# Kernel tuning notes

Measured on AMD Instinct MI355X. Metric: run time of the kernel, lower is better.

Reference implementation:

```python
import jax, jax.numpy as jnp
import numpy as np


def monarch_linear(x, w1, w2, bias, out_features):
    """Monarch structured linear: permute + block-diag + permute + block-diag.
    x: (B, n_in); w1: (k, q, p); w2: (l, s, r) with k*q == l*r.
    """
    b, n = x.shape
    k, q, p = w1.shape
    l, s, r = w2.shape
    n_ext = k * p
    if n_ext > n:  # preprocess: zero-pad input to in_features_extended
        x = jnp.pad(x, ((0, 0), (0, n_ext - n)))
    # first block-diagonal matmul: (B,k,p) x (k,q,p) -> (B,k,q)
    out1 = jnp.einsum('bkp,kqp->bkq', x.reshape(b, k, p), w1)
    # permutation: view (B, k*q) as (B, r, l) then transpose -> (B, l, r)
    out1 = out1.reshape(b, r, l).transpose(0, 2, 1)
    # second block-diagonal matmul: (B,l,r) x (l,s,r) -> (B,l,s)
    out2 = jnp.einsum('blr,lsr->bls', out1, w2)
    # final permutation: (B,l,s) -> (B,s,l) -> (B, s*l), then slice to out_features
    out = out2.transpose(0, 2, 1).reshape(b, s * l)[:, :out_features]
    return out + bias


def setup_inputs() -> dict:
    key = jax.random.key(0)
    ks = jax.random.split(key, 14)
    B = 65536
    specs = {
        'x': (B, 1, 28, 28),
        'fc1_w1': (15, 27, 53), 'fc1_w2': (15, 27, 27), 'fc1_b': (392,),
        'fc2_w1': (15, 9, 27), 'fc2_w2': (15, 9, 9), 'fc2_b': (128,),
        'fc3_w1': (15, 5, 9), 'fc3_w2': (15, 5, 5), 'fc3_b': (64,),
        'fc4_w1': (15, 1, 5), 'fc4_w2': (15, 1, 1), 'fc4_b': (10,),
    }
    out = {}
    for i, (name, shape) in enumerate(specs.items()):
        v = jax.random.normal(ks[i], shape, dtype=jnp.float32)
        if name != 'x':
            v = v * 0.1  # keep activations in a sane range through 4 layers
        out[name] = v
    return out


def reference(x, fc1_w1, fc1_w2, fc1_b, fc2_w1, fc2_w2, fc2_b,
              fc3_w1, fc3_w2, fc3_b, fc4_w1, fc4_w2, fc4_b):
    gelu = lambda t: jax.nn.gelu(t, approximate=False)  # torch F.gelu default = exact erf
    h = x.reshape(x.shape[0], -1)  # flatten (B,1,28,28) -> (B,784)
    h = gelu(monarch_linear(h, fc1_w1, fc1_w2, fc1_b, 392))
    h = gelu(monarch_linear(h, fc2_w1, fc2_w2, fc2_b, 128))
    h = gelu(monarch_linear(h, fc3_w1, fc3_w2, fc3_b, 64))
    h = monarch_linear(h, fc4_w1, fc4_w2, fc4_b, 10)
    return jax.nn.log_softmax(h, axis=1)
```

## Files before the change

kernel.cpp:

```cpp
#include <hip/hip_runtime.h>
#include <hip/hip_bf16.h>

typedef unsigned short u16;
typedef unsigned int   u32;

__device__ __forceinline__ float b2f(u16 v){ return __uint_as_float(((u32)v) << 16); }
__device__ __forceinline__ u16   f2b(float f){
  u32 u = __float_as_uint(f);
  u += 0x7fffu + ((u >> 16) & 1u);
  return (u16)(u >> 16);
}
__device__ __forceinline__ float gelu_exact(float x){
  return 0.5f * x * (1.0f + erff(x * 0.70710678118654752440f));
}

#define WTG_OFF   0
#define W2G_OFF   22720
#define W12G_OFF  34112
#define PREP_F    37952

__global__ __launch_bounds__(256) void k_prep(
    const float* __restrict__ w1, const float* __restrict__ w2,
    const float* __restrict__ w1_2, float* __restrict__ ws)
{
  int tid = blockIdx.x*256 + threadIdx.x;
  for (int e = tid; e < 15*54*28; e += gridDim.x*256){
    int kk = e / 1512, rem = e - kk*1512;
    int p = rem / 28, j = rem - p*28;
    ws[WTG_OFF + e] = (p < 53 && j < 27) ? w1[(kk*27 + j)*53 + p] : 0.0f;
  }
  for (int e = tid; e < 15*27*28; e += gridDim.x*256){
    int l = e / 756, rem = e - l*756;
    int s = rem / 28, r = rem - s*28;
    ws[W2G_OFF + e] = (r < 27) ? w2[(l*27 + s)*27 + r] : 0.0f;
  }
  for (int e = tid; e < 15*9*28; e += gridDim.x*256){
    int kk = e / 252, rem = e - kk*252;
    int j = rem / 28, p = rem - j*28;
    ws[W12G_OFF + e] = (p < 27) ? w1_2[(kk*9 + j)*27 + p] : 0.0f;
  }
}

__global__ __launch_bounds__(256, 5) void k_fc1a(
    const float* __restrict__ x, const float* __restrict__ wtg,
    u16* __restrict__ act, int base, int Bc)
{
  __shared__ u32 xsu[256*27];
  const int tid = threadIdx.x;
  const int k   = blockIdx.y;
  const int rowloc = blockIdx.x * 256;

  #pragma unroll 4
  for (int i = 0; i < 27; ++i){
    int e = i*256 + tid;
    int r = e / 27, c2 = e - r*27;
    int col = k*53 + 2*c2;
    const size_t rowoff = (size_t)(base + rowloc + r)*784;
    float v0 = 0.f, v1 = 0.f;
    if (col < 784) v0 = x[rowoff + col];
    if (2*c2+1 < 53 && col+1 < 784) v1 = x[rowoff + col + 1];
    xsu[e] = (u32)f2b(v0) | ((u32)f2b(v1) << 16);
  }
  __syncthreads();

  float acc[28];
  #pragma unroll
  for (int j = 0; j < 28; ++j) acc[j] = 0.0f;

  const float* __restrict__ wk = wtg + (size_t)k*1512;
  const u32* xrow = &xsu[tid*27];
  #pragma unroll
  for (int pp = 0; pp < 27; ++pp){
    const u32 xv2 = xrow[pp];
    const float x0 = __uint_as_float(xv2 << 16);
    const float x1 = __uint_as_float(xv2 & 0xffff0000u);
    const float4* wa = (const float4*)(wk + 56*pp);
    const float4* wb = (const float4*)(wk + 56*pp + 28);
    #pragma unroll
    for (int i = 0; i < 7; ++i){
      const float4 a = wa[i];
      const float4 b = wb[i];
      acc[4*i+0] = fmaf(a.x, x0, fmaf(b.x, x1, acc[4*i+0]));
      acc[4*i+1] = fmaf(a.y, x0, fmaf(b.y, x1, acc[4*i+1]));
      acc[4*i+2] = fmaf(a.z, x0, fmaf(b.z, x1, acc[4*i+2]));
      acc[4*i+3] = fmaf(a.w, x0, fmaf(b.w, x1, acc[4*i+3]));
    }
  }
  const int r0 = rowloc + tid;
  #pragma unroll
  for (int j = 0; j < 27; ++j)
    act[(size_t)(k*27 + j)*Bc + r0] = f2b(acc[j]);
}

__global__ __launch_bounds__(256) void k_fc1b(
    const float* __restrict__ w2g, const float* __restrict__ b1,
    u16* act, int Bc)
{
  const int tid = threadIdx.x;
  const int l   = blockIdx.y;
  const int row = blockIdx.x*256 + tid;
  const float* __restrict__ wl = w2g + (size_t)l*756;

  float t[28];
  #pragma unroll
  for (int r = 0; r < 27; ++r) t[r] = b2f(act[(size_t)(r*15 + l)*Bc + row]);
  t[27] = 0.0f;
  #pragma unroll
  for (int s = 0; s < 27; ++s){
    const float4* wp = (const float4*)(wl + s*28);
    float va = 0.f, vb = 0.f;
    #pragma unroll
    for (int i = 0; i < 7; ++i){
      const float4 w = wp[i];
      va = fmaf(w.x, t[4*i+0], va); vb = fmaf(w.y, t[4*i+1], vb);
      va = fmaf(w.z, t[4*i+2], va); vb = fmaf(w.w, t[4*i+3], vb);
    }
    const int m = s*15 + l;
    const float bb = (m < 392) ? b1[m] : 0.0f;
    const float h = (m < 392) ? gelu_exact(va + vb + bb) : 0.0f;
    act[(size_t)m*Bc + row] = f2b(h);
  }
}

__global__ __launch_bounds__(256) void k_fc2a(
    const u16* __restrict__ h1t, const float* __restrict__ w12g,
    u16* __restrict__ o2t, int Bc)
{
  const int tid = threadIdx.x;
  const int k   = blockIdx.y;
  const int row = blockIdx.x*256 + tid;
  const float* __restrict__ wk = w12g + (size_t)k*252;

  float hb[28];
  #pragma unroll
  for (int p = 0; p < 27; ++p) hb[p] = b2f(h1t[(size_t)(k*27 + p)*Bc + row]);
  hb[27] = 0.0f;
  #pragma unroll
  for (int j = 0; j < 9; ++j){
    const float4* wp = (const float4*)(wk + j*28);
    float va = 0.f, vb = 0.f;
    #pragma unroll
    for (int i = 0; i < 7; ++i){
      const float4 w = wp[i];
      va = fmaf(w.x, hb[4*i+0], va); vb = fmaf(w.y, hb[4*i+1], vb);
      va = fmaf(w.z, hb[4*i+2], va); vb = fmaf(w.w, hb[4*i+3], vb);
    }
    o2t[(size_t)(k*9 + j)*Bc + row] = f2b(va + vb);
  }
}

__global__ __launch_bounds__(256) void k_fc2b(
    const u16* __restrict__ o2t, const float* __restrict__ w2_2,
    const float* __restrict__ b2, u16* __restrict__ h2t, int Bc)
{
  const int tid = threadIdx.x;
  const int l   = blockIdx.y;
  const float* __restrict__ wl = w2_2 + (size_t)l*81;

  const int row = blockIdx.x*256 + tid;
  float t[9];
  #pragma unroll
  for (int r = 0; r < 9; ++r) t[r] = b2f(o2t[(size_t)(r*15 + l)*Bc + row]);
  #pragma unroll
  for (int s = 0; s < 9; ++s){
    float v = 0.f;
    #pragma unroll
    for (int r = 0; r < 9; ++r) v = fmaf(wl[s*9 + r], t[r], v);
    const int m = s*15 + l;
    float h = (m < 128) ? gelu_exact(v + b2[m < 128 ? m : 0]) : 0.0f;
    h2t[(size_t)m*Bc + row] = f2b(h);
  }
}

__global__ __launch_bounds__(256) void k_fc3a(
    const u16* __restrict__ h2t, const float* __restrict__ w1_3,
    u16* __restrict__ o3t, int Bc)
{
  const int tid = threadIdx.x;
  const int k   = blockIdx.y;
  const float* __restrict__ wk = w1_3 + (size_t)k*45;

  const int row = blockIdx.x*256 + tid;
  float hb[9];
  #pragma unroll
  for (int p = 0; p < 9; ++p) hb[p] = b2f(h2t[(size_t)(k*9 + p)*Bc + row]);
  #pragma unroll
  for (int j = 0; j < 5; ++j){
    float v = 0.f;
    #pragma unroll
    for (int p = 0; p < 9; ++p) v = fmaf(wk[j*9 + p], hb[p], v);
    o3t[(size_t)(k*5 + j)*Bc + row] = f2b(v);
  }
}

__global__ __launch_bounds__(256) void k_fc3b4(
    const u16* __restrict__ o3t,
    const float* __restrict__ w2_3, const float* __restrict__ b3,
    const float* __restrict__ w1_4, const float* __restrict__ w2_4, const float* __restrict__ b4,
    float* __restrict__ out, int base, int Bc)
{
  __shared__ float outS[256*10];
  const int tid = threadIdx.x;
  const int rloc = blockIdx.x*256 + tid;

  float sacc[10];
  #pragma unroll
  for (int c = 0; c < 10; ++c) sacc[c] = 0.0f;

  #pragma unroll
  for (int l = 0; l < 15; ++l){
    float t[5];
    #pragma unroll
    for (int r = 0; r < 5; ++r) t[r] = b2f(o3t[(size_t)(r*15 + l)*Bc + rloc]);
    #pragma unroll
    for (int s = 0; s < 5; ++s){
      const int m = s*15 + l;
      if (m < 50){
        const float* wp = w2_3 + (l*5 + s)*5;
        float v = 0.f;
        v = fmaf(wp[0], t[0], v); v = fmaf(wp[1], t[1], v);
        v = fmaf(wp[2], t[2], v); v = fmaf(wp[3], t[3], v);
        v = fmaf(wp[4], t[4], v);
        const float h = gelu_exact(v + b3[m]);
        const int c = m / 5, p = m - (m/5)*5;
        sacc[c] = fmaf(h, w1_4[c*5 + p], sacc[c]);
      }
    }
  }
  float v[10];
  #pragma unroll
  for (int c = 0; c < 10; ++c) v[c] = fmaf(sacc[c], w2_4[c], b4[c]);

  float mx = v[0];
  #pragma unroll
  for (int c = 1; c < 10; ++c) mx = fmaxf(mx, v[c]);
  float sum = 0.f;
  #pragma unroll
  for (int c = 0; c < 10; ++c) sum += expf(v[c] - mx);
  const float lse = mx + logf(sum);
  #pragma unroll
  for (int c = 0; c < 10; ++c) outS[tid*10 + c] = v[c] - lse;
  __syncthreads();
  const size_t blockOut = (size_t)(base + blockIdx.x*256) * 10;
  #pragma unroll
  for (int i = 0; i < 10; ++i){
    int e = i*256 + tid;
    out[blockOut + e] = outS[e];
  }
}

extern "C" void kernel_launch(void* const* d_in, const int* in_sizes, int n_in,
                              void* d_out, int out_size, void* d_ws, size_t ws_size,
                              hipStream_t stream)
{
  const float* x     = (const float*)d_in[0];
  const float* f1w1  = (const float*)d_in[1];
  const float* f1w2  = (const float*)d_in[2];
  const float* f1b   = (const float*)d_in[3];
  const float* f2w1  = (const float*)d_in[4];
  const float* f2w2  = (const float*)d_in[5];
  const float* f2b   = (const float*)d_in[6];
  const float* f3w1  = (const float*)d_in[7];
  const float* f3w2  = (const float*)d_in[8];
  const float* f3b   = (const float*)d_in[9];
  const float* f4w1  = (const float*)d_in[10];
  const float* f4w2  = (const float*)d_in[11];
  const float* f4b   = (const float*)d_in[12];
  const int B = in_sizes[0] / 784;
  (void)n_in; (void)out_size;

  const size_t prepBytes = (size_t)PREP_F * sizeof(float);
  float* wsF  = (float*)d_ws;
  u16*  wsAct = (u16*)((char*)d_ws + prepBytes);

  k_prep<<<dim3(32), 256, 0, stream>>>(f1w1, f1w2, f2w1, wsF);

  const float* wtg  = wsF + WTG_OFF;
  const float* w2g  = wsF + W2G_OFF;
  const float* w12g = wsF + W12G_OFF;

  const size_t perRow = 750 * sizeof(u16);
  int Rc = B;
  if (ws_size - prepBytes < (size_t)B * perRow){
    size_t rows = (ws_size - prepBytes) / perRow;
    Rc = (int)(rows & ~(size_t)511);
    if (Rc < 512) Rc = 512;
  }
  for (int base = 0; base < B; base += Rc){
    const int Bc = (B - base < Rc) ? (B - base) : Rc;
    u16* act = wsAct;
    u16* o2t = act + (size_t)405 * Bc;
    u16* h2t = o2t + (size_t)135 * Bc;
    u16* o3t = h2t + (size_t)135 * Bc;
    k_fc1a<<<dim3(Bc/256, 15), 256, 0, stream>>>(x, wtg, act, base, Bc);
    k_fc1b<<<dim3(Bc/256, 15), 256, 0, stream>>>(w2g, f1b, act, Bc);
    k_fc2a<<<dim3(Bc/256, 15), 256, 0, stream>>>(act, w12g, o2t, Bc);
    k_fc2b<<<dim3(Bc/256, 15), 256, 0, stream>>>(o2t, f2w2, f2b, h2t, Bc);
    k_fc3a<<<dim3(Bc/256, 15), 256, 0, stream>>>(h2t, f3w1, o3t, Bc);
    k_fc3b4<<<dim3(Bc/256), 256, 0, stream>>>(o3t, f3w2, f3b,
                                              f4w1, f4w2, f4b, (float*)d_out, base, Bc);
  }
}
```

Measured before the change: 462.1 us.

## Fuse fc2b, fc3a and fc3b/fc4 tail into a single per-row kernel

Result: slower. 505.7 us (+9.4%).

```diff
diff --git a/kernel.cpp b/kernel.cpp
--- a/kernel.cpp
+++ b/kernel.cpp
@@ -10,6 +10,7 @@
   u += 0x7fffu + ((u >> 16) & 1u);
   return (u16)(u >> 16);
 }
+__device__ __forceinline__ float bfrt(float f){ return b2f(f2b(f)); }
 __device__ __forceinline__ float gelu_exact(float x){
   return 0.5f * x * (1.0f + erff(x * 0.70710678118654752440f));
 }
@@ -149,59 +150,46 @@
   }
 }
 
-__global__ __launch_bounds__(256) void k_fc2b(
-    const u16* __restrict__ o2t, const float* __restrict__ w2_2,
-    const float* __restrict__ b2, u16* __restrict__ h2t, int Bc)
-{
-  const int tid = threadIdx.x;
-  const int l   = blockIdx.y;
-  const float* __restrict__ wl = w2_2 + (size_t)l*81;
-
-  const int row = blockIdx.x*256 + tid;
-  float t[9];
-  #pragma unroll
-  for (int r = 0; r < 9; ++r) t[r] = b2f(o2t[(size_t)(r*15 + l)*Bc + row]);
-  #pragma unroll
-  for (int s = 0; s < 9; ++s){
-    float v = 0.f;
-    #pragma unroll
-    for (int r = 0; r < 9; ++r) v = fmaf(wl[s*9 + r], t[r], v);
-    const int m = s*15 + l;
-    float h = (m < 128) ? gelu_exact(v + b2[m < 128 ? m : 0]) : 0.0f;
-    h2t[(size_t)m*Bc + row] = f2b(h);
-  }
-}
-
-__global__ __launch_bounds__(256) void k_fc3a(
-    const u16* __restrict__ h2t, const float* __restrict__ w1_3,
-    u16* __restrict__ o3t, int Bc)
-{
-  const int tid = threadIdx.x;
-  const int k   = blockIdx.y;
-  const float* __restrict__ wk = w1_3 + (size_t)k*45;
-
-  const int row = blockIdx.x*256 + tid;
-  float hb[9];
-  #pragma unroll
-  for (int p = 0; p < 9; ++p) hb[p] = b2f(h2t[(size_t)(k*9 + p)*Bc + row]);
-  #pragma unroll
-  for (int j = 0; j < 5; ++j){
-    float v = 0.f;
-    #pragma unroll
-    for (int p = 0; p < 9; ++p) v = fmaf(wk[j*9 + p], hb[p], v);
-    o3t[(size_t)(k*5 + j)*Bc + row] = f2b(v);
-  }
-}
-
-__global__ __launch_bounds__(256) void k_fc3b4(
-    const u16* __restrict__ o3t,
+__global__ __launch_bounds__(256) void k_tail(
+    const u16* __restrict__ o2t,
+    const float* __restrict__ w2_2, const float* __restrict__ b2,
+    const float* __restrict__ w1_3,
     const float* __restrict__ w2_3, const float* __restrict__ b3,
     const float* __restrict__ w1_4, const float* __restrict__ w2_4, const float* __restrict__ b4,
     float* __restrict__ out, int base, int Bc)
 {
   __shared__ float outS[256*10];
   const int tid = threadIdx.x;
-  const int rloc = blockIdx.x*256 + tid;
+  const int row = blockIdx.x*256 + tid;
+
+  float h2[135];
+  #pragma unroll
+  for (int l = 0; l < 15; ++l){
+    float t[9];
+    #pragma unroll
+    for (int r = 0; r < 9; ++r) t[r] = b2f(o2t[(size_t)(r*15 + l)*Bc + row]);
+    #pragma unroll
+    for (int s = 0; s < 9; ++s){
+      const int m = s*15 + l;
+      float v = 0.f;
+      #pragma unroll
+      for (int r = 0; r < 9; ++r) v = fmaf(w2_2[l*81 + s*9 + r], t[r], v);
+      const float h = (m < 128) ? gelu_exact(v + b2[m < 128 ? m : 0]) : 0.0f;
+      h2[m] = bfrt(h);
+    }
+  }
+
+  float o3[75];
+  #pragma unroll
+  for (int k2 = 0; k2 < 15; ++k2){
+    #pragma unroll
+    for (int j = 0; j < 5; ++j){
+      float v = 0.f;
+      #pragma unroll
+      for (int p = 0; p < 9; ++p) v = fmaf(w1_3[k2*45 + j*9 + p], h2[k2*9 + p], v);
+      o3[k2*5 + j] = bfrt(v);
+    }
+  }
 
   float sacc[10];
   #pragma unroll
@@ -211,7 +199,7 @@
   for (int l = 0; l < 15; ++l){
     float t[5];
     #pragma unroll
-    for (int r = 0; r < 5; ++r) t[r] = b2f(o3t[(size_t)(r*15 + l)*Bc + rloc]);
+    for (int r = 0; r < 5; ++r) t[r] = o3[r*15 + l];
     #pragma unroll
     for (int s = 0; s < 5; ++s){
       const int m = s*15 + l;
@@ -279,7 +267,7 @@
   const float* w2g  = wsF + W2G_OFF;
   const float* w12g = wsF + W12G_OFF;
 
-  const size_t perRow = 750 * sizeof(u16);
+  const size_t perRow = 540 * sizeof(u16);
   int Rc = B;
   if (ws_size - prepBytes < (size_t)B * perRow){
     size_t rows = (ws_size - prepBytes) / perRow;
@@ -290,14 +278,11 @@
     const int Bc = (B - base < Rc) ? (B - base) : Rc;
     u16* act = wsAct;
     u16* o2t = act + (size_t)405 * Bc;
-    u16* h2t = o2t + (size_t)135 * Bc;
-    u16* o3t = h2t + (size_t)135 * Bc;
     k_fc1a<<<dim3(Bc/256, 15), 256, 0, stream>>>(x, wtg, act, base, Bc);
     k_fc1b<<<dim3(Bc/256, 15), 256, 0, stream>>>(w2g, f1b, act, Bc);
     k_fc2a<<<dim3(Bc/256, 15), 256, 0, stream>>>(act, w12g, o2t, Bc);
-    k_fc2b<<<dim3(Bc/256, 15), 256, 0, stream>>>(o2t, f2w2, f2b, h2t, Bc);
-    k_fc3a<<<dim3(Bc/256, 15), 256, 0, stream>>>(h2t, f3w1, o3t, Bc);
-    k_fc3b4<<<dim3(Bc/256), 256, 0, stream>>>(o3t, f3w2, f3b,
-                                              f4w1, f4w2, f4b, (float*)d_out, base, Bc);
-  }
-}
+    k_tail<<<dim3(Bc/256), 256, 0, stream>>>(o2t, f2w2, f2b, f3w1,
+                                             f3w2, f3b, f4w1, f4w2, f4b,
+                                             (float*)d_out, base, Bc);
+  }
+}
```

## Use bf16 MFMA with hi/lo weight split for fc1 first block-diagonal matmul

Applied to the files above, without the earlier changes.

Result: slower. 484.9 us (+4.9%).

```diff
diff --git a/kernel.cpp b/kernel.cpp
--- a/kernel.cpp
+++ b/kernel.cpp
@@ -3,6 +3,8 @@
 
 typedef unsigned short u16;
 typedef unsigned int   u32;
+typedef __attribute__((ext_vector_type(8))) short short8;
+typedef __attribute__((ext_vector_type(4))) float f32x4;
 
 __device__ __forceinline__ float b2f(u16 v){ return __uint_as_float(((u32)v) << 16); }
 __device__ __forceinline__ u16   f2b(float f){
@@ -14,82 +16,110 @@
   return 0.5f * x * (1.0f + erff(x * 0.70710678118654752440f));
 }
 
-#define WTG_OFF   0
-#define W2G_OFF   22720
-#define W12G_OFF  34112
-#define PREP_F    37952
+#define W2G_OFF   0
+#define W12G_OFF  11340
+#define PREP_F    15120
+#define WFRAG_U16 61440
+#define PREP_BYTES (PREP_F*4 + WFRAG_U16*2)
 
 __global__ __launch_bounds__(256) void k_prep(
     const float* __restrict__ w1, const float* __restrict__ w2,
-    const float* __restrict__ w1_2, float* __restrict__ ws)
+    const float* __restrict__ w1_2, float* __restrict__ wsF,
+    u16* __restrict__ wfrag)
 {
   int tid = blockIdx.x*256 + threadIdx.x;
-  for (int e = tid; e < 15*54*28; e += gridDim.x*256){
-    int kk = e / 1512, rem = e - kk*1512;
-    int p = rem / 28, j = rem - p*28;
-    ws[WTG_OFF + e] = (p < 53 && j < 27) ? w1[(kk*27 + j)*53 + p] : 0.0f;
-  }
   for (int e = tid; e < 15*27*28; e += gridDim.x*256){
     int l = e / 756, rem = e - l*756;
     int s = rem / 28, r = rem - s*28;
-    ws[W2G_OFF + e] = (r < 27) ? w2[(l*27 + s)*27 + r] : 0.0f;
+    wsF[W2G_OFF + e] = (r < 27) ? w2[(l*27 + s)*27 + r] : 0.0f;
   }
   for (int e = tid; e < 15*9*28; e += gridDim.x*256){
     int kk = e / 252, rem = e - kk*252;
     int j = rem / 28, p = rem - j*28;
-    ws[W12G_OFF + e] = (p < 27) ? w1_2[(kk*9 + j)*27 + p] : 0.0f;
-  }
-}
-
-__global__ __launch_bounds__(256, 5) void k_fc1a(
-    const float* __restrict__ x, const float* __restrict__ wtg,
+    wsF[W12G_OFF + e] = (p < 27) ? w1_2[(kk*9 + j)*27 + p] : 0.0f;
+  }
+  for (int e = tid; e < 30720; e += gridDim.x*256){
+    int k  = e / 2048, rem = e - k*2048;
+    int s  = rem / 1024; rem -= s*1024;
+    int ct = rem / 512;  int sl = rem - ct*512;
+    int lane = sl / 8, i = sl - lane*8;
+    int p = s*32 + (lane >> 4)*8 + i;
+    int j = ct*16 + (lane & 15);
+    float wv = (p < 53 && j < 27) ? w1[(k*27 + j)*53 + p] : 0.0f;
+    u16 hi = f2b(wv);
+    u16 lo = f2b(wv - b2f(hi));
+    int bidx = (k*2 + s)*2 + ct;
+    wfrag[bidx*1024 + sl]       = hi;
+    wfrag[bidx*1024 + 512 + sl] = lo;
+  }
+}
+
+__global__ __launch_bounds__(256, 4) void k_fc1a(
+    const float* __restrict__ x, const u16* __restrict__ wfrag,
     u16* __restrict__ act, int base, int Bc)
 {
-  __shared__ u32 xsu[256*27];
+  __shared__ __align__(16) u16 xs[256*72];
   const int tid = threadIdx.x;
   const int k   = blockIdx.y;
   const int rowloc = blockIdx.x * 256;
 
+  u32* xsu = (u32*)xs;
   #pragma unroll 4
-  for (int i = 0; i < 27; ++i){
+  for (int i = 0; i < 36; ++i){
     int e = i*256 + tid;
-    int r = e / 27, c2 = e - r*27;
+    int r = e / 36, c2 = e - r*36;
     int col = k*53 + 2*c2;
     const size_t rowoff = (size_t)(base + rowloc + r)*784;
     float v0 = 0.f, v1 = 0.f;
-    if (col < 784) v0 = x[rowoff + col];
+    if (2*c2   < 53 && col   < 784) v0 = x[rowoff + col];
     if (2*c2+1 < 53 && col+1 < 784) v1 = x[rowoff + col + 1];
     xsu[e] = (u32)f2b(v0) | ((u32)f2b(v1) << 16);
   }
   __syncthreads();
 
-  float acc[28];
-  #pragma unroll
-  for (int j = 0; j < 28; ++j) acc[j] = 0.0f;
-
-  const float* __restrict__ wk = wtg + (size_t)k*1512;
-  const u32* xrow = &xsu[tid*27];
-  #pragma unroll
-  for (int pp = 0; pp < 27; ++pp){
-    const u32 xv2 = xrow[pp];
-    const float x0 = __uint_as_float(xv2 << 16);
-    const float x1 = __uint_as_float(xv2 & 0xffff0000u);
-    const float4* wa = (const float4*)(wk + 56*pp);
-    const float4* wb = (const float4*)(wk + 56*pp + 28);
-    #pragma unroll
-    for (int i = 0; i < 7; ++i){
-      const float4 a = wa[i];
-      const float4 b = wb[i];
-      acc[4*i+0] = fmaf(a.x, x0, fmaf(b.x, x1, acc[4*i+0]));
-      acc[4*i+1] = fmaf(a.y, x0, fmaf(b.y, x1, acc[4*i+1]));
-      acc[4*i+2] = fmaf(a.z, x0, fmaf(b.z, x1, acc[4*i+2]));
-      acc[4*i+3] = fmaf(a.w, x0, fmaf(b.w, x1, acc[4*i+3]));
-    }
-  }
-  const int r0 = rowloc + tid;
-  #pragma unroll
-  for (int j = 0; j < 27; ++j)
-    act[(size_t)(k*27 + j)*Bc + r0] = f2b(acc[j]);
+  const int lane = tid & 63;
+  const int w    = tid >> 6;
+  const int lrow = lane & 15;
+  const int lgrp = lane >> 4;
+
+  f32x4 acc[4][2];
+  #pragma unroll
+  for (int t = 0; t < 4; ++t){
+    #pragma unroll
+    for (int c = 0; c < 2; ++c) acc[t][c] = (f32x4){0.f,0.f,0.f,0.f};
+  }
+
+  #pragma unroll
+  for (int s = 0; s < 2; ++s){
+    const u16* fb = wfrag + ((k*2 + s)*2)*1024;
+    const short8 bh0 = *(const short8*)(fb +         lane*8);
+    const short8 bl0 = *(const short8*)(fb +  512 +  lane*8);
+    const short8 bh1 = *(const short8*)(fb + 1024 +  lane*8);
+    const short8 bl1 = *(const short8*)(fb + 1536 +  lane*8);
+    #pragma unroll
+    for (int t = 0; t < 4; ++t){
+      const short8 av = *(const short8*)&xs[(w*64 + t*16 + lrow)*72 + s*32 + lgrp*8];
+      acc[t][0] = __builtin_amdgcn_mfma_f32_16x16x32_bf16(av, bh0, acc[t][0], 0, 0, 0);
+      acc[t][0] = __builtin_amdgcn_mfma_f32_16x16x32_bf16(av, bl0, acc[t][0], 0, 0, 0);
+      acc[t][1] = __builtin_amdgcn_mfma_f32_16x16x32_bf16(av, bh1, acc[t][1], 0, 0, 0);
+      acc[t][1] = __builtin_amdgcn_mfma_f32_16x16x32_bf16(av, bl1, acc[t][1], 0, 0, 0);
+    }
+  }
+
+  #pragma unroll
+  for (int ct = 0; ct < 2; ++ct){
+    const int col = ct*16 + lrow;
+    if (col < 27){
+      #pragma unroll
+      for (int t = 0; t < 4; ++t){
+        const f32x4 a = acc[t][ct];
+        u32 lo = (u32)f2b(a.x) | ((u32)f2b(a.y) << 16);
+        u32 hi = (u32)f2b(a.z) | ((u32)f2b(a.w) << 16);
+        const size_t idx = (size_t)(k*27 + col)*Bc + rowloc + w*64 + t*16 + lgrp*4;
+        *(uint2*)&act[idx] = make_uint2(lo, hi);
+      }
+    }
+  }
 }
 
 __global__ __launch_bounds__(256) void k_fc1b(
@@ -269,20 +299,19 @@
   const int B = in_sizes[0] / 784;
   (void)n_in; (void)out_size;
 
-  const size_t prepBytes = (size_t)PREP_F * sizeof(float);
-  float* wsF  = (float*)d_ws;
-  u16*  wsAct = (u16*)((char*)d_ws + prepBytes);
-
-  k_prep<<<dim3(32), 256, 0, stream>>>(f1w1, f1w2, f2w1, wsF);
-
-  const float* wtg  = wsF + WTG_OFF;
+  float* wsF   = (float*)d_ws;
+  u16*  wfrag  = (u16*)((char*)d_ws + PREP_F*4);
+  u16*  wsAct  = (u16*)((char*)d_ws + PREP_BYTES);
+
+  k_prep<<<dim3(32), 256, 0, stream>>>(f1w1, f1w2, f2w1, wsF, wfrag);
+
   const float* w2g  = wsF + W2G_OFF;
   const float* w12g = wsF + W12G_OFF;
 
   const size_t perRow = 750 * sizeof(u16);
   int Rc = B;
-  if (ws_size - prepBytes < (size_t)B * perRow){
-    size_t rows = (ws_size - prepBytes) / perRow;
+  if (ws_size - PREP_BYTES < (size_t)B * perRow){
+    size_t rows = (ws_size - PREP_BYTES) / perRow;
     Rc = (int)(rows & ~(size_t)511);
     if (Rc < 512) Rc = 512;
   }
@@ -292,7 +321,7 @@
     u16* o2t = act + (size_t)405 * Bc;
     u16* h2t = o2t + (size_t)135 * Bc;
     u16* o3t = h2t + (size_t)135 * Bc;
-    k_fc1a<<<dim3(Bc/256, 15), 256, 0, stream>>>(x, wtg, act, base, Bc);
+    k_fc1a<<<dim3(Bc/256, 15), 256, 0, stream>>>(x, wfrag, act, base, Bc);
     k_fc1b<<<dim3(Bc/256, 15), 256, 0, stream>>>(w2g, f1b, act, Bc);
     k_fc2a<<<dim3(Bc/256, 15), 256, 0, stream>>>(act, w12g, o2t, Bc);
     k_fc2b<<<dim3(Bc/256, 15), 256, 0, stream>>>(o2t, f2w2, f2b, h2t, Bc);
```
